# Kernel tuning notes

Hardware: AMD Instinct MI355X
Metric: run time of the kernel (lower is better)

Reference implementation:

```python
import jax, jax.numpy as jnp
import numpy as np

N = 50000
E = 600000
HID = 128
NF = 128
NG = 50
CUTOFF = 10.0
LOG2 = float(np.log(2.0))


def ssp(x):
    # shifted softplus: softplus(x) - log(2)
    return jax.nn.softplus(x) - LOG2


def setup_inputs() -> dict:
    key = jax.random.key(0)
    ks = jax.random.split(key, 12)
    h = jax.random.normal(ks[0], (N, HID), dtype=jnp.float32)
    edge_index = jax.random.randint(ks[1], (2, E), 0, N)
    edge_weight = jax.random.uniform(ks[2], (E,), dtype=jnp.float32) * CUTOFF
    edge_attr = jax.random.normal(ks[3], (E, NG), dtype=jnp.float32)
    # parameters (torch Linear weight layout: [out, in])
    def xavier(k, shape):
        fan_out, fan_in = shape
        lim = np.sqrt(6.0 / (fan_in + fan_out))
        return jax.random.uniform(k, shape, jnp.float32, -lim, lim)
    mlp_w0 = xavier(ks[4], (NF, NG))
    mlp_b0 = jnp.zeros((NF,), jnp.float32)
    mlp_w2 = xavier(ks[5], (NF, NF))
    mlp_b2 = jnp.zeros((NF,), jnp.float32)
    lin1_w = xavier(ks[6], (NF, HID))
    lin2_w = xavier(ks[7], (HID, NF))
    lin2_b = jnp.zeros((HID,), jnp.float32)
    lin_w = xavier(ks[8], (HID, HID))
    lin_b = jnp.zeros((HID,), jnp.float32)
    return {
        "h": h, "edge_index": edge_index, "edge_weight": edge_weight,
        "edge_attr": edge_attr, "mlp_w0": mlp_w0, "mlp_b0": mlp_b0,
        "mlp_w2": mlp_w2, "mlp_b2": mlp_b2, "lin1_w": lin1_w,
        "lin2_w": lin2_w, "lin2_b": lin2_b, "lin_w": lin_w, "lin_b": lin_b,
    }


def reference(h, edge_index, edge_weight, edge_attr, mlp_w0, mlp_b0,
              mlp_w2, mlp_b2, lin1_w, lin2_w, lin2_b, lin_w, lin_b):
    src, dst = edge_index[0], edge_index[1]
    # CFConv
    h1 = h @ lin1_w.T                                   # [N, NF]
    c = 0.5 * (jnp.cos(edge_weight / CUTOFF * jnp.pi) + 1.0)  # [E]
    W = ssp(edge_attr @ mlp_w0.T + mlp_b0) @ mlp_w2.T + mlp_b2  # [E, NF]
    message = c[:, None] * (W * h1[src])                # [E, NF]
    agg = jax.ops.segment_sum(message, dst, num_segments=h.shape[0])
    h2 = (h1 + agg) @ lin2_w.T + lin2_b                 # [N, HID]
    # InteractionBlock tail
    return ssp(h2) @ lin_w.T + lin_b
```

## Files before the change

kernel.cpp:

```cpp
#include <hip/hip_runtime.h>
#include <math.h>

#define HID 128
#define NF  128
#define NG  50

typedef unsigned short ushort_t;
typedef unsigned short us8 __attribute__((ext_vector_type(8)));
typedef unsigned short us4 __attribute__((ext_vector_type(4)));
typedef unsigned short us2 __attribute__((ext_vector_type(2)));
typedef __bf16 bf16x8 __attribute__((ext_vector_type(8)));
typedef float f32x4 __attribute__((ext_vector_type(4)));

__device__ inline float ssp_fast(float x) {
    float t = __builtin_amdgcn_exp2f(fabsf(x) * -1.4426950408889634f);
    float l = __builtin_amdgcn_logf(1.0f + t);
    return fmaxf(x, 0.0f) + 0.6931471805599453f * (l - 1.0f);
}

__device__ inline ushort_t f2bf(float f) {
    return __builtin_bit_cast(ushort_t, (__bf16)f);
}
__device__ inline float bf2f(ushort_t h) {
    unsigned u = ((unsigned)h) << 16;
    return __builtin_bit_cast(float, u);
}

__device__ inline void gload16(const void* g, void* l) {
    __builtin_amdgcn_global_load_lds(
        (const __attribute__((address_space(1))) void*)g,
        (__attribute__((address_space(3))) void*)l, 16, 0, 0);
}

__global__ void prep_count(const int* __restrict__ dstI, int* counts,
                           int* __restrict__ slot,
                           const float* __restrict__ lin1_w,
                           const float* __restrict__ lin2_w,
                           const float* __restrict__ lin_w,
                           const float* __restrict__ mlp_w0,
                           const float* __restrict__ mlp_w2,
                           ushort_t* __restrict__ l1b,
                           ushort_t* __restrict__ l2b,
                           ushort_t* __restrict__ lfb,
                           ushort_t* __restrict__ w0g,
                           ushort_t* __restrict__ w2g,
                           int* __restrict__ sidecar_pad,
                           int E, int nsp) {
    int idx = blockIdx.x * 256 + threadIdx.x;
    if (idx < E) {
        slot[idx] = atomicAdd(&counts[dstI[idx]], 1);
        return;
    }
    int k = idx - E;
    if (k < 49152) {
        int m = k >> 14, i = k & 16383;
        int o = i >> 7, kk = i & 127;
        const float* s = (m == 0) ? lin1_w : (m == 1) ? lin2_w : lin_w;
        ushort_t*    d = (m == 0) ? l1b    : (m == 1) ? l2b    : lfb;
        d[o * 128 + (kk ^ ((o & 7) << 3))] = f2bf(s[i]);
    } else if (k < 57344) {
        int i = k - 49152;
        int o = i >> 6, kk = i & 63;
        float v = (kk < 50) ? mlp_w0[o * 50 + kk] : 0.f;
        w0g[i] = f2bf(v);
    } else if (k < 73728) {
        int i = k - 57344;
        w2g[i] = f2bf(mlp_w2[i]);
    } else if (k < 73728 + nsp) {
        sidecar_pad[k - 73728] = 0;
    }
}

__global__ __launch_bounds__(1024) void scan1(const int* __restrict__ counts,
                                              int* __restrict__ off,
                                              int* __restrict__ bsum, int n) {
    __shared__ int s[1024];
    int t = threadIdx.x, g = blockIdx.x * 1024 + t;
    int c = (g < n) ? counts[g] : 0;
    s[t] = c;
    __syncthreads();
    for (int d = 1; d < 1024; d <<= 1) {
        int v = (t >= d) ? s[t - d] : 0;
        __syncthreads();
        s[t] += v;
        __syncthreads();
    }
    if (g < n) off[g] = s[t] - c;
    if (t == 1023) bsum[blockIdx.x] = s[1023];
}

__global__ __launch_bounds__(1024, 4) void h1_and_permute(
    const float* __restrict__ A, const ushort_t* __restrict__ Wb,
    ushort_t* __restrict__ h1b, float* __restrict__ aggz, int n_rows, int ngrid,
    const int* __restrict__ srcI, const int* __restrict__ dstI,
    const int* __restrict__ slot, const int* __restrict__ off,
    const int* __restrict__ bsum, int nsb, const float* __restrict__ ew,
    int4* __restrict__ sidecar, int E)
{
    __shared__ ushort_t a_s[128 * 128];
    __shared__ ushort_t w_s[128 * 128];
    const int tid = threadIdx.x;

    if (blockIdx.x >= ngrid) {
        int* cs  = (int*)a_s;
        int* cse = (int*)a_s + 64;
        int own = 0;
        if (tid < 64) {
            own = (tid < nsb) ? bsum[tid] : 0;
            cs[tid] = own;
        }
        __syncthreads();
        for (int d = 1; d < 64; d <<= 1) {
            int v = 0;
            if (tid < 64 && tid >= d) v = cs[tid - d];
            __syncthreads();
            if (tid < 64) cs[tid] += v;
            __syncthreads();
        }
        if (tid < 64) cse[tid] = cs[tid] - own;
        __syncthreads();

        int e = (blockIdx.x - ngrid) * 1024 + tid;
        if (e < E) {
            int d = dstI[e];
            int p = off[d] + cse[d >> 10] + slot[e];
            float cw = 0.5f * (__builtin_amdgcn_cosf(ew[e] * 0.05f) + 1.0f);
            sidecar[p] = make_int4(srcI[e], d, __float_as_int(cw), e);
        }
        return;
    }

    const int n0 = blockIdx.x * 128;
    const int lane = tid & 63, wid = tid >> 6;

    #pragma unroll
    for (int i = 0; i < 2; ++i) {
        int cid = wid * 2 + i;
        gload16(Wb + cid * 512 + lane * 8, w_s + cid * 512);
    }
    {
        int r = tid >> 3, q = tid & 7;
        int n = n0 + r;
        float vals[16];
        if (n < n_rows) {
            #pragma unroll
            for (int j = 0; j < 4; ++j) {
                f32x4 v = ((const f32x4*)A)[(size_t)n * 32 + q * 4 + j];
                #pragma unroll
                for (int x = 0; x < 4; ++x) vals[j * 4 + x] = v[x];
            }
        } else {
            #pragma unroll
            for (int x = 0; x < 16; ++x) vals[x] = 0.f;
        }
        int sw = (r & 7) << 3;
        #pragma unroll
        for (int hh = 0; hh < 2; ++hh) {
            us8 pk;
            #pragma unroll
            for (int x = 0; x < 8; ++x) pk[x] = f2bf(vals[hh * 8 + x]);
            *(us8*)&a_s[r * 128 + ((q * 16 + hh * 8) ^ sw)] = pk;
        }
    }
    __syncthreads();

    const int og = (wid >> 2) * 32;
    const int rg = (wid & 3) * 32;
    const int lm = lane & 15, lh = lane >> 4;

    f32x4 acc[2][2];
    #pragma unroll
    for (int mt = 0; mt < 2; ++mt)
        #pragma unroll
        for (int nt = 0; nt < 2; ++nt) acc[mt][nt] = (f32x4){0.f, 0.f, 0.f, 0.f};

    #pragma unroll
    for (int ks = 0; ks < 4; ++ks) {
        int k8 = ks * 32 + lh * 8;
        bf16x8 af[2], wf[2];
        #pragma unroll
        for (int mt = 0; mt < 2; ++mt) {
            int m = rg + mt * 16 + lm;
            af[mt] = __builtin_bit_cast(bf16x8,
                *(const us8*)&a_s[m * 128 + (k8 ^ ((m & 7) << 3))]);
        }
        #pragma unroll
        for (int nt = 0; nt < 2; ++nt) {
            int n = og + nt * 16 + lm;
            wf[nt] = __builtin_bit_cast(bf16x8,
                *(const us8*)&w_s[n * 128 + (k8 ^ ((n & 7) << 3))]);
        }
        #pragma unroll
        for (int mt = 0; mt < 2; ++mt)
            #pragma unroll
            for (int nt = 0; nt < 2; ++nt)
                acc[mt][nt] = __builtin_amdgcn_mfma_f32_16x16x32_bf16(
                    af[mt], wf[nt], acc[mt][nt], 0, 0, 0);
    }

    #pragma unroll
    for (int nt = 0; nt < 2; ++nt) {
        int outc = og + nt * 16 + lm;
        #pragma unroll
        for (int mt = 0; mt < 2; ++mt) {
            int rbase = rg + mt * 16 + lh * 4;
            #pragma unroll
            for (int j = 0; j < 4; ++j) {
                int n = n0 + rbase + j;
                if (n < n_rows) {
                    h1b[(size_t)n * 128 + outc] = f2bf(acc[mt][nt][j]);
                    aggz[(size_t)n * 128 + outc] = 0.f;
                }
            }
        }
    }
}

__global__ __launch_bounds__(1024, 4) void gemm23_fused(
    const ushort_t* __restrict__ h1b, const float* __restrict__ agg,
    const ushort_t* __restrict__ l2b, const float* __restrict__ b2,
    const ushort_t* __restrict__ lfb, const float* __restrict__ lb,
    float* __restrict__ outF, int n_rows)
{
    __shared__ ushort_t a_s[128 * 128];
    __shared__ ushort_t w_s[128 * 128];
    const int tid = threadIdx.x;
    const int n0 = blockIdx.x * 128;
    const int lane = tid & 63, wid = tid >> 6;

    #pragma unroll
    for (int i = 0; i < 2; ++i) {
        int cid = wid * 2 + i;
        gload16(l2b + cid * 512 + lane * 8, w_s + cid * 512);
    }
    {
        int r = tid >> 3, q = tid & 7;
        int n = n0 + r;
        float vals[16];
        if (n < n_rows) {
            us8 hb0 = *(const us8*)&h1b[(size_t)n * 128 + q * 16];
            us8 hb1 = *(const us8*)&h1b[(size_t)n * 128 + q * 16 + 8];
            #pragma unroll
            for (int j = 0; j < 4; ++j) {
                f32x4 av = ((const f32x4*)agg)[(size_t)n * 32 + q * 4 + j];
                #pragma unroll
                for (int x = 0; x < 4; ++x) {
                    int c = j * 4 + x;
                    float hv = bf2f(c < 8 ? hb0[c] : hb1[c - 8]);
                    vals[c] = hv + av[x];
                }
            }
        } else {
            #pragma unroll
            for (int x = 0; x < 16; ++x) vals[x] = 0.f;
        }
        int sw = (r & 7) << 3;
        #pragma unroll
        for (int hh = 0; hh < 2; ++hh) {
            us8 pk;
            #pragma unroll
            for (int x = 0; x < 8; ++x) pk[x] = f2bf(vals[hh * 8 + x]);
            *(us8*)&a_s[r * 128 + ((q * 16 + hh * 8) ^ sw)] = pk;
        }
    }
    __syncthreads();

    const int og = (wid >> 2) * 32;
    const int rg = (wid & 3) * 32;
    const int lm = lane & 15, lh = lane >> 4;

    f32x4 acc[2][2];
    #pragma unroll
    for (int mt = 0; mt < 2; ++mt)
        #pragma unroll
        for (int nt = 0; nt < 2; ++nt) acc[mt][nt] = (f32x4){0.f, 0.f, 0.f, 0.f};
    #pragma unroll
    for (int ks = 0; ks < 4; ++ks) {
        int k8 = ks * 32 + lh * 8;
        bf16x8 af[2], wf[2];
        #pragma unroll
        for (int mt = 0; mt < 2; ++mt) {
            int m = rg + mt * 16 + lm;
            af[mt] = __builtin_bit_cast(bf16x8,
                *(const us8*)&a_s[m * 128 + (k8 ^ ((m & 7) << 3))]);
        }
        #pragma unroll
        for (int nt = 0; nt < 2; ++nt) {
            int n = og + nt * 16 + lm;
            wf[nt] = __builtin_bit_cast(bf16x8,
                *(const us8*)&w_s[n * 128 + (k8 ^ ((n & 7) << 3))]);
        }
        #pragma unroll
        for (int mt = 0; mt < 2; ++mt)
            #pragma unroll
            for (int nt = 0; nt < 2; ++nt)
                acc[mt][nt] = __builtin_amdgcn_mfma_f32_16x16x32_bf16(
                    af[mt], wf[nt], acc[mt][nt], 0, 0, 0);
    }
    __syncthreads();

    #pragma unroll
    for (int i = 0; i < 2; ++i) {
        int cid = wid * 2 + i;
        gload16(lfb + cid * 512 + lane * 8, w_s + cid * 512);
    }
    #pragma unroll
    for (int nt = 0; nt < 2; ++nt) {
        int outc = og + nt * 16 + lm;
        float bv = b2[outc];
        #pragma unroll
        for (int mt = 0; mt < 2; ++mt) {
            int rbase = rg + mt * 16 + lh * 4;
            #pragma unroll
            for (int j = 0; j < 4; ++j) {
                int r = rbase + j;
                a_s[r * 128 + (outc ^ ((r & 7) << 3))] =
                    f2bf(ssp_fast(acc[mt][nt][j] + bv));
            }
        }
    }
    __syncthreads();

    f32x4 acc2[2][2];
    #pragma unroll
    for (int mt = 0; mt < 2; ++mt)
        #pragma unroll
        for (int nt = 0; nt < 2; ++nt) acc2[mt][nt] = (f32x4){0.f, 0.f, 0.f, 0.f};
    #pragma unroll
    for (int ks = 0; ks < 4; ++ks) {
        int k8 = ks * 32 + lh * 8;
        bf16x8 af[2], wf[2];
        #pragma unroll
        for (int mt = 0; mt < 2; ++mt) {
            int m = rg + mt * 16 + lm;
            af[mt] = __builtin_bit_cast(bf16x8,
                *(const us8*)&a_s[m * 128 + (k8 ^ ((m & 7) << 3))]);
        }
        #pragma unroll
        for (int nt = 0; nt < 2; ++nt) {
            int n = og + nt * 16 + lm;
            wf[nt] = __builtin_bit_cast(bf16x8,
                *(const us8*)&w_s[n * 128 + (k8 ^ ((n & 7) << 3))]);
        }
        #pragma unroll
        for (int mt = 0; mt < 2; ++mt)
            #pragma unroll
            for (int nt = 0; nt < 2; ++nt)
                acc2[mt][nt] = __builtin_amdgcn_mfma_f32_16x16x32_bf16(
                    af[mt], wf[nt], acc2[mt][nt], 0, 0, 0);
    }

    #pragma unroll
    for (int nt = 0; nt < 2; ++nt) {
        int outc = og + nt * 16 + lm;
        float bv = lb[outc];
        #pragma unroll
        for (int mt = 0; mt < 2; ++mt) {
            int rbase = rg + mt * 16 + lh * 4;
            #pragma unroll
            for (int j = 0; j < 4; ++j) {
                int n = n0 + rbase + j;
                if (n < n_rows)
                    outF[(size_t)n * 128 + outc] = acc2[mt][nt][j] + bv;
            }
        }
    }
}

__global__ __launch_bounds__(256, 6) void edge_fused(
    const float* __restrict__ ea, const int4* __restrict__ sidecar,
    const ushort_t* __restrict__ w0g, const ushort_t* __restrict__ w2g,
    const float* __restrict__ b0g, const float* __restrict__ b2g,
    const ushort_t* __restrict__ h1b, float* __restrict__ agg, int E)
{
    __shared__ __align__(16) char blob[25344];
    ushort_t* ea_s = (ushort_t*)blob;
    ushort_t* u_s  = (ushort_t*)(blob + 8192);
    ushort_t* m_sb = (ushort_t*)blob;
    float* cws = (float*)(blob + 24576);
    int* srcs  = (int*)(blob + 24832);
    int* dsts  = (int*)(blob + 25088);

    const int tid = threadIdx.x;
    const int p0 = blockIdx.x * 64;
    const int lane = tid & 63, wid = tid >> 6;
    const int out0w = wid * 32;
    const int lm = lane & 15, lh = lane >> 4;

    {
        int r = tid >> 2, q = tid & 3;
        int p = p0 + r;
        int eidx = ((const int*)sidecar)[(size_t)p * 4 + 3];
        const float2* row2 = (const float2*)(ea + (size_t)eidx * 50);
        us8 pk0 = {0, 0, 0, 0, 0, 0, 0, 0};
        us8 pk1 = {0, 0, 0, 0, 0, 0, 0, 0};
        if (q < 3) {
            #pragma unroll
            for (int j = 0; j < 4; ++j) {
                float2 f = row2[q * 8 + j];
                pk0[2 * j]     = f2bf(f.x);
                pk0[2 * j + 1] = f2bf(f.y);
            }
            #pragma unroll
            for (int j = 0; j < 4; ++j) {
                float2 f = row2[q * 8 + 4 + j];
                pk1[2 * j]     = f2bf(f.x);
                pk1[2 * j + 1] = f2bf(f.y);
            }
        } else {
            float2 f = row2[24];
            pk0[0] = f2bf(f.x);
            pk0[1] = f2bf(f.y);
        }
        int sw = (r & 7) << 3;
        *(us8*)&ea_s[r * 64 + ((q * 16)     ^ sw)] = pk0;
        *(us8*)&ea_s[r * 64 + ((q * 16 + 8) ^ sw)] = pk1;
    }
    if (tid < 64) {
        int4 sc = sidecar[p0 + tid];
        srcs[tid] = sc.x; dsts[tid] = sc.y; cws[tid] = __int_as_float(sc.z);
    }

    bf16x8 w0f[2][2];
    #pragma unroll
    for (int ks = 0; ks < 2; ++ks)
        #pragma unroll
        for (int mt = 0; mt < 2; ++mt) {
            int n = out0w + mt * 16 + lm;
            w0f[ks][mt] = __builtin_bit_cast(bf16x8,
                *(const us8*)&w0g[n * 64 + ks * 32 + lh * 8]);
        }
    __syncthreads();

    f32x4 acc1[2][4];
    #pragma unroll
    for (int mt = 0; mt < 2; ++mt)
        #pragma unroll
        for (int nt = 0; nt < 4; ++nt) acc1[mt][nt] = (f32x4){0.f, 0.f, 0.f, 0.f};
    #pragma unroll
    for (int ks = 0; ks < 2; ++ks) {
        int k8 = ks * 32 + lh * 8;
        #pragma unroll
        for (int nt = 0; nt < 4; ++nt) {
            int e = nt * 16 + lm;
            bf16x8 be = __builtin_bit_cast(bf16x8,
                *(const us8*)&ea_s[e * 64 + (k8 ^ ((e & 7) << 3))]);
            #pragma unroll
            for (int mt = 0; mt < 2; ++mt)
                acc1[mt][nt] = __builtin_amdgcn_mfma_f32_16x16x32_bf16(
                    w0f[ks][mt], be, acc1[mt][nt], 0, 0, 0);
        }
    }

    #pragma unroll
    for (int mt = 0; mt < 2; ++mt) {
        int out0 = out0w + mt * 16 + lh * 4;
        f32x4 b0v = *(const f32x4*)&b0g[out0];
        #pragma unroll
        for (int nt = 0; nt < 4; ++nt) {
            int e = nt * 16 + lm;
            us4 pk;
            #pragma unroll
            for (int j = 0; j < 4; ++j)
                pk[j] = f2bf(ssp_fast(acc1[mt][nt][j] + b0v[j]));
            *(us4*)&u_s[e * 128 + (out0 ^ ((e & 7) << 3))] = pk;
        }
    }

    bf16x8 w2f[4][2];
    #pragma unroll
    for (int ks = 0; ks < 4; ++ks)
        #pragma unroll
        for (int mt = 0; mt < 2; ++mt) {
            int n = out0w + mt * 16 + lm;
            w2f[ks][mt] = __builtin_bit_cast(bf16x8,
                *(const us8*)&w2g[n * 128 + ks * 32 + lh * 8]);
        }
    __syncthreads();

    f32x4 acc2[2][4];
    #pragma unroll
    for (int mt = 0; mt < 2; ++mt)
        #pragma unroll
        for (int nt = 0; nt < 4; ++nt) acc2[mt][nt] = (f32x4){0.f, 0.f, 0.f, 0.f};
    #pragma unroll
    for (int ks = 0; ks < 4; ++ks) {
        int k8 = ks * 32 + lh * 8;
        #pragma unroll
        for (int nt = 0; nt < 4; ++nt) {
            int e = nt * 16 + lm;
            bf16x8 be = __builtin_bit_cast(bf16x8,
                *(const us8*)&u_s[e * 128 + (k8 ^ ((e & 7) << 3))]);
            #pragma unroll
            for (int mt = 0; mt < 2; ++mt)
                acc2[mt][nt] = __builtin_amdgcn_mfma_f32_16x16x32_bf16(
                    w2f[ks][mt], be, acc2[mt][nt], 0, 0, 0);
        }
    }
    __syncthreads();

    #pragma unroll
    for (int mt = 0; mt < 2; ++mt) {
        int out0 = out0w + mt * 16 + lh * 4;
        f32x4 b2v = *(const f32x4*)&b2g[out0];
        #pragma unroll
        for (int nt = 0; nt < 4; ++nt) {
            int e = nt * 16 + lm;
            float cvv = cws[e];
            us4 pk;
            #pragma unroll
            for (int j = 0; j < 4; ++j)
                pk[j] = f2bf(cvv * (acc2[mt][nt][j] + b2v[j]));
            *(us4*)&m_sb[e * 128 + (out0 ^ ((e & 7) << 2))] = pk;
        }
    }

    const int i0 = wid * 16;
    us2 h1r[16];
    #pragma unroll
    for (int j = 0; j < 16; ++j) {
        int s = srcs[i0 + j];
        h1r[j] = *(const us2*)&h1b[(size_t)s * 128 + lane * 2];
    }
    __syncthreads();

    {
        const int cp = lane;
        float sx = 0.f, sy = 0.f;
        int prev = dsts[i0];
        #pragma unroll
        for (int j = 0; j < 16; ++j) {
            int i = i0 + j;
            int d = dsts[i];
            us2 wv = *(const us2*)&m_sb[i * 128 + ((cp * 2) ^ ((i & 7) << 2))];
            if (d != prev) {
                atomicAdd(&agg[(size_t)prev * 128 + cp * 2], sx);
                atomicAdd(&agg[(size_t)prev * 128 + cp * 2 + 1], sy);
                sx = 0.f; sy = 0.f; prev = d;
            }
            sx += bf2f(wv[0]) * bf2f(h1r[j][0]);
            sy += bf2f(wv[1]) * bf2f(h1r[j][1]);
        }
        atomicAdd(&agg[(size_t)prev * 128 + cp * 2], sx);
        atomicAdd(&agg[(size_t)prev * 128 + cp * 2 + 1], sy);
    }
}

extern "C" void kernel_launch(void* const* d_in, const int* in_sizes, int n_in,
                              void* d_out, int out_size, void* d_ws, size_t ws_size,
                              hipStream_t stream) {
    const float* h       = (const float*)d_in[0];
    const int*   ei      = (const int*)  d_in[1];
    const float* ew      = (const float*)d_in[2];
    const float* ea      = (const float*)d_in[3];
    const float* mlp_w0  = (const float*)d_in[4];
    const float* mlp_b0  = (const float*)d_in[5];
    const float* mlp_w2  = (const float*)d_in[6];
    const float* mlp_b2  = (const float*)d_in[7];
    const float* lin1_w  = (const float*)d_in[8];
    const float* lin2_w  = (const float*)d_in[9];
    const float* lin2_b  = (const float*)d_in[10];
    const float* lin_w   = (const float*)d_in[11];
    const float* lin_b   = (const float*)d_in[12];
    float* out = (float*)d_out;
    float* ws  = (float*)d_ws;

    const int N = in_sizes[0] / HID;
    const int E = in_sizes[2];
    const int PADE = (E + 63) & ~63;
    const int NODE_PAD = (N + 256) & ~255;
    const int NSB = (N + 1023) / 1024;

    float* agg   = ws;
    ushort_t* h1b = (ushort_t*)(agg + (size_t)N * 128);
    ushort_t* l1b = (ushort_t*)((float*)h1b + (size_t)N * 64);
    ushort_t* l2b = l1b + 16384;
    ushort_t* lfb = l2b + 16384;
    ushort_t* w0g = lfb + 16384;
    ushort_t* w2g = w0g + 8192;
    int* counts  = (int*)(w2g + 16384);
    int* off     = counts + NODE_PAD;
    int* bsum    = off + NODE_PAD;
    int* slot    = bsum + 64;
    int4* sidecar = (int4*)(slot + E);

    const int* srcI = ei;
    const int* dstI = ei + E;

    hipMemsetAsync(counts, 0, (size_t)NODE_PAD * 4, stream);

    const int nsp = (PADE - E) * 4;
    int total_threads = E + 73728 + nsp;
    prep_count<<<(total_threads + 255) / 256, 256, 0, stream>>>(
        dstI, counts, slot, lin1_w, lin2_w, lin_w, mlp_w0, mlp_w2,
        l1b, l2b, lfb, w0g, w2g, (int*)(sidecar + E), E, nsp);

    scan1<<<NSB, 1024, 0, stream>>>(counts, off, bsum, N);

    int ngrid = (N + 127) / 128;
    int pb    = (E + 1023) / 1024;
    h1_and_permute<<<ngrid + pb, 1024, 0, stream>>>(
        h, l1b, h1b, agg, N, ngrid,
        srcI, dstI, slot, off, bsum, NSB, ew, sidecar, E);

    edge_fused<<<PADE / 64, 256, 0, stream>>>(ea, sidecar, w0g, w2g,
                                              mlp_b0, mlp_b2, h1b, agg, E);

    gemm23_fused<<<ngrid, 1024, 0, stream>>>(h1b, agg, l2b, lin2_b,
                                             lfb, lin_b, out, N);
}
```

Before: 180.8 us.

## Process two 64-edge tiles per block with register prefetch of second tile

The edge kernel now handles 128 edges per block as two 64-edge sub-tiles. The second tile's edge_attr rows are loaded into registers up front and written to shared memory after the first tile's first GEMM, hiding gather latency. The W0 fragments are reused across both tiles. The message buffer moves to its own shared region so the input buffer can be refilled. This costs more registers and shared memory, lowers the launch-bounds occupancy target from 6 to 5, and halves the grid size.

```diff
diff --git a/kernel.cpp b/kernel.cpp
--- a/kernel.cpp
+++ b/kernel.cpp
@@ -367,56 +367,69 @@
     }
 }
 
-__global__ __launch_bounds__(256, 6) void edge_fused(
+__global__ __launch_bounds__(256, 5) void edge_fused(
     const float* __restrict__ ea, const int4* __restrict__ sidecar,
     const ushort_t* __restrict__ w0g, const ushort_t* __restrict__ w2g,
     const float* __restrict__ b0g, const float* __restrict__ b2g,
     const ushort_t* __restrict__ h1b, float* __restrict__ agg, int E)
 {
-    __shared__ __align__(16) char blob[25344];
+    __shared__ __align__(16) char blob[26112];
     ushort_t* ea_s = (ushort_t*)blob;
     ushort_t* u_s  = (ushort_t*)(blob + 8192);
-    ushort_t* m_sb = (ushort_t*)blob;
+    ushort_t* m_sb = (ushort_t*)(blob + 8192);
     float* cws = (float*)(blob + 24576);
-    int* srcs  = (int*)(blob + 24832);
-    int* dsts  = (int*)(blob + 25088);
+    int* srcs  = (int*)(blob + 25088);
+    int* dsts  = (int*)(blob + 25600);
 
     const int tid = threadIdx.x;
-    const int p0 = blockIdx.x * 64;
+    const int p0 = blockIdx.x * 128;
     const int lane = tid & 63, wid = tid >> 6;
     const int out0w = wid * 32;
     const int lm = lane & 15, lh = lane >> 4;
-
+    const int r = tid >> 2, q = tid & 3;
+    const int sw = (r & 7) << 3;
+
+    float2 v0[8], v1[8];
     {
-        int r = tid >> 2, q = tid & 3;
-        int p = p0 + r;
-        int eidx = ((const int*)sidecar)[(size_t)p * 4 + 3];
-        const float2* row2 = (const float2*)(ea + (size_t)eidx * 50);
-        us8 pk0 = {0, 0, 0, 0, 0, 0, 0, 0};
-        us8 pk1 = {0, 0, 0, 0, 0, 0, 0, 0};
+        int e0 = ((const int*)sidecar)[(size_t)(p0 + r) * 4 + 3];
+        int e1 = ((const int*)sidecar)[(size_t)(p0 + 64 + r) * 4 + 3];
+        const float2* r0 = (const float2*)(ea + (size_t)e0 * 50);
+        const float2* r1 = (const float2*)(ea + (size_t)e1 * 50);
         if (q < 3) {
             #pragma unroll
-            for (int j = 0; j < 4; ++j) {
-                float2 f = row2[q * 8 + j];
-                pk0[2 * j]     = f2bf(f.x);
-                pk0[2 * j + 1] = f2bf(f.y);
-            }
-            #pragma unroll
-            for (int j = 0; j < 4; ++j) {
-                float2 f = row2[q * 8 + 4 + j];
-                pk1[2 * j]     = f2bf(f.x);
-                pk1[2 * j + 1] = f2bf(f.y);
-            }
+            for (int j = 0; j < 8; ++j) v0[j] = r0[q * 8 + j];
+            #pragma unroll
+            for (int j = 0; j < 8; ++j) v1[j] = r1[q * 8 + j];
         } else {
-            float2 f = row2[24];
-            pk0[0] = f2bf(f.x);
-            pk0[1] = f2bf(f.y);
-        }
-        int sw = (r & 7) << 3;
+            v0[0] = r0[24]; v1[0] = r1[24];
+            #pragma unroll
+            for (int j = 1; j < 8; ++j) {
+                v0[j] = make_float2(0.f, 0.f);
+                v1[j] = make_float2(0.f, 0.f);
+            }
+        }
+    }
+    {
+        us8 pk0, pk1;
+        #pragma unroll
+        for (int x = 0; x < 4; ++x) {
+            pk0[2 * x]     = f2bf(v0[x].x);
+            pk0[2 * x + 1] = f2bf(v0[x].y);
+            pk1[2 * x]     = f2bf(v0[4 + x].x);
+            pk1[2 * x + 1] = f2bf(v0[4 + x].y);
+        }
         *(us8*)&ea_s[r * 64 + ((q * 16)     ^ sw)] = pk0;
         *(us8*)&ea_s[r * 64 + ((q * 16 + 8) ^ sw)] = pk1;
     }
-    if (tid < 64) {
+    us8 g1a, g1b;
+    #pragma unroll
+    for (int x = 0; x < 4; ++x) {
+        g1a[2 * x]     = f2bf(v1[x].x);
+        g1a[2 * x + 1] = f2bf(v1[x].y);
+        g1b[2 * x]     = f2bf(v1[4 + x].x);
+        g1b[2 * x + 1] = f2bf(v1[4 + x].y);
+    }
+    if (tid < 128) {
         int4 sc = sidecar[p0 + tid];
         srcs[tid] = sc.x; dsts[tid] = sc.y; cws[tid] = __int_as_float(sc.z);
     }
@@ -432,117 +445,125 @@
         }
     __syncthreads();
 
-    f32x4 acc1[2][4];
-    #pragma unroll
-    for (int mt = 0; mt < 2; ++mt)
-        #pragma unroll
-        for (int nt = 0; nt < 4; ++nt) acc1[mt][nt] = (f32x4){0.f, 0.f, 0.f, 0.f};
-    #pragma unroll
-    for (int ks = 0; ks < 2; ++ks) {
-        int k8 = ks * 32 + lh * 8;
-        #pragma unroll
-        for (int nt = 0; nt < 4; ++nt) {
-            int e = nt * 16 + lm;
-            bf16x8 be = __builtin_bit_cast(bf16x8,
-                *(const us8*)&ea_s[e * 64 + (k8 ^ ((e & 7) << 3))]);
-            #pragma unroll
-            for (int mt = 0; mt < 2; ++mt)
-                acc1[mt][nt] = __builtin_amdgcn_mfma_f32_16x16x32_bf16(
-                    w0f[ks][mt], be, acc1[mt][nt], 0, 0, 0);
-        }
-    }
-
-    #pragma unroll
-    for (int mt = 0; mt < 2; ++mt) {
-        int out0 = out0w + mt * 16 + lh * 4;
-        f32x4 b0v = *(const f32x4*)&b0g[out0];
-        #pragma unroll
-        for (int nt = 0; nt < 4; ++nt) {
-            int e = nt * 16 + lm;
-            us4 pk;
-            #pragma unroll
-            for (int j = 0; j < 4; ++j)
-                pk[j] = f2bf(ssp_fast(acc1[mt][nt][j] + b0v[j]));
-            *(us4*)&u_s[e * 128 + (out0 ^ ((e & 7) << 3))] = pk;
-        }
-    }
-
-    bf16x8 w2f[4][2];
-    #pragma unroll
-    for (int ks = 0; ks < 4; ++ks)
-        #pragma unroll
-        for (int mt = 0; mt < 2; ++mt) {
-            int n = out0w + mt * 16 + lm;
-            w2f[ks][mt] = __builtin_bit_cast(bf16x8,
-                *(const us8*)&w2g[n * 128 + ks * 32 + lh * 8]);
-        }
-    __syncthreads();
-
-    f32x4 acc2[2][4];
-    #pragma unroll
-    for (int mt = 0; mt < 2; ++mt)
-        #pragma unroll
-        for (int nt = 0; nt < 4; ++nt) acc2[mt][nt] = (f32x4){0.f, 0.f, 0.f, 0.f};
-    #pragma unroll
-    for (int ks = 0; ks < 4; ++ks) {
-        int k8 = ks * 32 + lh * 8;
-        #pragma unroll
-        for (int nt = 0; nt < 4; ++nt) {
-            int e = nt * 16 + lm;
-            bf16x8 be = __builtin_bit_cast(bf16x8,
-                *(const us8*)&u_s[e * 128 + (k8 ^ ((e & 7) << 3))]);
-            #pragma unroll
-            for (int mt = 0; mt < 2; ++mt)
-                acc2[mt][nt] = __builtin_amdgcn_mfma_f32_16x16x32_bf16(
-                    w2f[ks][mt], be, acc2[mt][nt], 0, 0, 0);
-        }
-    }
-    __syncthreads();
-
-    #pragma unroll
-    for (int mt = 0; mt < 2; ++mt) {
-        int out0 = out0w + mt * 16 + lh * 4;
-        f32x4 b2v = *(const f32x4*)&b2g[out0];
-        #pragma unroll
-        for (int nt = 0; nt < 4; ++nt) {
-            int e = nt * 16 + lm;
-            float cvv = cws[e];
-            us4 pk;
-            #pragma unroll
-            for (int j = 0; j < 4; ++j)
-                pk[j] = f2bf(cvv * (acc2[mt][nt][j] + b2v[j]));
-            *(us4*)&m_sb[e * 128 + (out0 ^ ((e & 7) << 2))] = pk;
-        }
-    }
-
-    const int i0 = wid * 16;
-    us2 h1r[16];
-    #pragma unroll
-    for (int j = 0; j < 16; ++j) {
-        int s = srcs[i0 + j];
-        h1r[j] = *(const us2*)&h1b[(size_t)s * 128 + lane * 2];
-    }
-    __syncthreads();
-
-    {
-        const int cp = lane;
-        float sx = 0.f, sy = 0.f;
-        int prev = dsts[i0];
+    #pragma unroll
+    for (int t = 0; t < 2; ++t) {
+        f32x4 acc1[2][4];
+        #pragma unroll
+        for (int mt = 0; mt < 2; ++mt)
+            #pragma unroll
+            for (int nt = 0; nt < 4; ++nt) acc1[mt][nt] = (f32x4){0.f, 0.f, 0.f, 0.f};
+        #pragma unroll
+        for (int ks = 0; ks < 2; ++ks) {
+            int k8 = ks * 32 + lh * 8;
+            #pragma unroll
+            for (int nt = 0; nt < 4; ++nt) {
+                int e = nt * 16 + lm;
+                bf16x8 be = __builtin_bit_cast(bf16x8,
+                    *(const us8*)&ea_s[e * 64 + (k8 ^ ((e & 7) << 3))]);
+                #pragma unroll
+                for (int mt = 0; mt < 2; ++mt)
+                    acc1[mt][nt] = __builtin_amdgcn_mfma_f32_16x16x32_bf16(
+                        w0f[ks][mt], be, acc1[mt][nt], 0, 0, 0);
+            }
+        }
+        __syncthreads();
+        if (t == 0) {
+            *(us8*)&ea_s[r * 64 + ((q * 16)     ^ sw)] = g1a;
+            *(us8*)&ea_s[r * 64 + ((q * 16 + 8) ^ sw)] = g1b;
+        }
+
+        #pragma unroll
+        for (int mt = 0; mt < 2; ++mt) {
+            int out0 = out0w + mt * 16 + lh * 4;
+            f32x4 b0v = *(const f32x4*)&b0g[out0];
+            #pragma unroll
+            for (int nt = 0; nt < 4; ++nt) {
+                int e = nt * 16 + lm;
+                us4 pk;
+                #pragma unroll
+                for (int j = 0; j < 4; ++j)
+                    pk[j] = f2bf(ssp_fast(acc1[mt][nt][j] + b0v[j]));
+                *(us4*)&u_s[e * 128 + (out0 ^ ((e & 7) << 3))] = pk;
+            }
+        }
+
+        bf16x8 w2f[4][2];
+        #pragma unroll
+        for (int ks = 0; ks < 4; ++ks)
+            #pragma unroll
+            for (int mt = 0; mt < 2; ++mt) {
+                int n = out0w + mt * 16 + lm;
+                w2f[ks][mt] = __builtin_bit_cast(bf16x8,
+                    *(const us8*)&w2g[n * 128 + ks * 32 + lh * 8]);
+            }
+        __syncthreads();
+
+        f32x4 acc2[2][4];
+        #pragma unroll
+        for (int mt = 0; mt < 2; ++mt)
+            #pragma unroll
+            for (int nt = 0; nt < 4; ++nt) acc2[mt][nt] = (f32x4){0.f, 0.f, 0.f, 0.f};
+        #pragma unroll
+        for (int ks = 0; ks < 4; ++ks) {
+            int k8 = ks * 32 + lh * 8;
+            #pragma unroll
+            for (int nt = 0; nt < 4; ++nt) {
+                int e = nt * 16 + lm;
+                bf16x8 be = __builtin_bit_cast(bf16x8,
+                    *(const us8*)&u_s[e * 128 + (k8 ^ ((e & 7) << 3))]);
+                #pragma unroll
+                for (int mt = 0; mt < 2; ++mt)
+                    acc2[mt][nt] = __builtin_amdgcn_mfma_f32_16x16x32_bf16(
+                        w2f[ks][mt], be, acc2[mt][nt], 0, 0, 0);
+            }
+        }
+        __syncthreads();
+
+        #pragma unroll
+        for (int mt = 0; mt < 2; ++mt) {
+            int out0 = out0w + mt * 16 + lh * 4;
+            f32x4 b2v = *(const f32x4*)&b2g[out0];
+            #pragma unroll
+            for (int nt = 0; nt < 4; ++nt) {
+                int e = nt * 16 + lm;
+                float cvv = cws[t * 64 + e];
+                us4 pk;
+                #pragma unroll
+                for (int j = 0; j < 4; ++j)
+                    pk[j] = f2bf(cvv * (acc2[mt][nt][j] + b2v[j]));
+                *(us4*)&m_sb[e * 128 + (out0 ^ ((e & 7) << 2))] = pk;
+            }
+        }
+
+        const int i0 = wid * 16;
+        us2 h1r[16];
         #pragma unroll
         for (int j = 0; j < 16; ++j) {
-            int i = i0 + j;
-            int d = dsts[i];
-            us2 wv = *(const us2*)&m_sb[i * 128 + ((cp * 2) ^ ((i & 7) << 2))];
-            if (d != prev) {
-                atomicAdd(&agg[(size_t)prev * 128 + cp * 2], sx);
-                atomicAdd(&agg[(size_t)prev * 128 + cp * 2 + 1], sy);
-                sx = 0.f; sy = 0.f; prev = d;
-            }
-            sx += bf2f(wv[0]) * bf2f(h1r[j][0]);
-            sy += bf2f(wv[1]) * bf2f(h1r[j][1]);
-        }
-        atomicAdd(&agg[(size_t)prev * 128 + cp * 2], sx);
-        atomicAdd(&agg[(size_t)prev * 128 + cp * 2 + 1], sy);
+            int s = srcs[t * 64 + i0 + j];
+            h1r[j] = *(const us2*)&h1b[(size_t)s * 128 + lane * 2];
+        }
+        __syncthreads();
+
+        {
+            const int cp = lane;
+            float sx = 0.f, sy = 0.f;
+            int prev = dsts[t * 64 + i0];
+            #pragma unroll
+            for (int j = 0; j < 16; ++j) {
+                int i = i0 + j;
+                int d = dsts[t * 64 + i];
+                us2 wv = *(const us2*)&m_sb[i * 128 + ((cp * 2) ^ ((i & 7) << 2))];
+                if (d != prev) {
+                    atomicAdd(&agg[(size_t)prev * 128 + cp * 2], sx);
+                    atomicAdd(&agg[(size_t)prev * 128 + cp * 2 + 1], sy);
+                    sx = 0.f; sy = 0.f; prev = d;
+                }
+                sx += bf2f(wv[0]) * bf2f(h1r[j][0]);
+                sy += bf2f(wv[1]) * bf2f(h1r[j][1]);
+            }
+            atomicAdd(&agg[(size_t)prev * 128 + cp * 2], sx);
+            atomicAdd(&agg[(size_t)prev * 128 + cp * 2 + 1], sy);
+        }
     }
 }
 
@@ -567,7 +588,7 @@
 
     const int N = in_sizes[0] / HID;
     const int E = in_sizes[2];
-    const int PADE = (E + 63) & ~63;
+    const int PADE = (E + 127) & ~127;
     const int NODE_PAD = (N + 256) & ~255;
     const int NSB = (N + 1023) / 1024;
 
@@ -603,8 +624,8 @@
         h, l1b, h1b, agg, N, ngrid,
         srcI, dstI, slot, off, bsum, NSB, ew, sidecar, E);
 
-    edge_fused<<<PADE / 64, 256, 0, stream>>>(ea, sidecar, w0g, w2g,
-                                              mlp_b0, mlp_b2, h1b, agg, E);
+    edge_fused<<<PADE / 128, 256, 0, stream>>>(ea, sidecar, w0g, w2g,
+                                               mlp_b0, mlp_b2, h1b, agg, E);
 
     gemm23_fused<<<ngrid, 1024, 0, stream>>>(h1b, agg, l2b, lin2_b,
                                              lfb, lin_b, out, N);
```

Result: slower. 206.0 us (+13.9%).
